# Performance work log

Measured on AMD Instinct MI355X. Metric: run time of the kernel, lower is better.

Reference implementation:

```python
import jax, jax.numpy as jnp
import numpy as np

NUM_CLASSES = 100000   # vocab (input_dim of the layer)
DIM = 256              # embedding dim (output_dim of the layer)
BATCH = 256
NUM_TRUE = 1024        # hardcoded num_true in call()
NUM_SAMPLED = 16384    # hardcoded num_sampled in call()
LOG_RANGE = float(np.log(NUM_CLASSES + 1.0))


def _sample_log_uniform_unique(rng, n, range_max):
    # Mimics tf log_uniform_candidate_sampler with unique=True: rejection-sample
    # from P(c) ~ log((c+2)/(c+1)) until n unique ids are collected.
    seen = {}
    log_range = np.log(range_max + 1.0)
    while len(seen) < n:
        u = rng.uniform(0.0, log_range, size=2 * n)
        ids = np.minimum(np.floor(np.exp(u) - 1.0).astype(np.int64), range_max - 1)
        for v in ids.tolist():
            if len(seen) >= n:
                break
            seen[v] = None
    return np.fromiter(seen.keys(), dtype=np.int64, count=n)


def setup_inputs() -> dict:
    key = jax.random.key(0)
    k1, k2, k3, k4 = jax.random.split(key, 4)
    inputs = jax.random.normal(k1, (BATCH, DIM), jnp.float32)
    # Original inits w/b to zeros; use small random values for a non-degenerate baseline.
    w = jax.random.normal(k2, (NUM_CLASSES, DIM), jnp.float32) * 0.02
    b = jax.random.normal(k3, (NUM_CLASSES,), jnp.float32) * 0.02
    labels = jax.random.randint(k4, (BATCH, NUM_TRUE), 0, NUM_CLASSES, dtype=jnp.int32)
    rng = np.random.default_rng(0)
    sampled = jnp.asarray(_sample_log_uniform_unique(rng, NUM_SAMPLED, NUM_CLASSES), jnp.int32)
    return {"inputs": inputs, "w": w, "b": b, "labels": labels, "sampled": sampled}


def _log_uniform_prob(ids):
    idf = ids.astype(jnp.float32)
    return jnp.log((idf + 2.0) / (idf + 1.0)) / LOG_RANGE


def _expected_count(ids):
    # P(id appears among NUM_SAMPLED unique candidates) = 1 - (1-p)^NUM_SAMPLED
    p = _log_uniform_prob(ids)
    return -jnp.expm1(NUM_SAMPLED * jnp.log1p(-p))


def _sigmoid_xent(logits, target):
    # numerically stable sigmoid cross-entropy, target is a scalar label value
    return jnp.maximum(logits, 0.0) - logits * target + jnp.log1p(jnp.exp(-jnp.abs(logits)))


def reference(inputs, w, b, labels, sampled):
    # true logits: per-example dot with each true class row  [B, T]
    true_w = w[labels]                                    # [B, T, D] gather
    true_logits = jnp.einsum('bd,btd->bt', inputs, true_w) + b[labels]
    true_logits = true_logits - jnp.log(_expected_count(labels))
    # sampled logits: shared candidate set  [B, S]
    sampled_logits = inputs @ w[sampled].T + b[sampled]
    sampled_logits = sampled_logits - jnp.log(_expected_count(sampled))
    # NCE targets: 1/num_true for true classes, 0 for sampled; sum over columns
    true_xent = _sigmoid_xent(true_logits, 1.0 / NUM_TRUE)
    sampled_xent = _sigmoid_xent(sampled_logits, 0.0)
    return true_xent.sum(axis=1) + sampled_xent.sum(axis=1)   # [B]
```

## Files before the change

kernel.cpp:

```cpp
#include <hip/hip_runtime.h>
#include <hip/hip_bf16.h>

#define NUM_CLASSES 100000
#define DIM 256
#define BATCH 256
#define NUM_TRUE 1024
#define NUM_SAMPLED 16384
#define LOG_RANGE 11.51293546492023f
#define INV_LOG_RANGE (1.0f / LOG_RANGE)

#define SBLOCKS 512
#define TBLOCKS 2048

typedef __bf16 bf16x8 __attribute__((ext_vector_type(8)));
typedef float  f32x4  __attribute__((ext_vector_type(4)));

static __device__ __forceinline__ unsigned short f2bf(float f) {
    unsigned int u = __float_as_uint(f);
    unsigned int lsb = (u >> 16) & 1u;
    u += 0x7fffu + lsb;
    return (unsigned short)(u >> 16);
}

static __device__ __forceinline__ float neg_log_ec_fast(int id) {
    float idf = (float)id;
    float e = 1.0f / (idf + 1.0f);
    float p = log1pf(e) * INV_LOG_RANGE;
    float q = p * (1.0f + 0.5f * p + 0.3333333f * p * p);
    float ec = 1.0f - __expf(-(float)NUM_SAMPLED * q);
    return -__logf(ec);
}

static __device__ __forceinline__ float dot4(float4 a, float4 b) {
    return fmaf(a.x, b.x, fmaf(a.y, b.y, fmaf(a.z, b.z, a.w * b.w)));
}

__global__ __launch_bounds__(256) void conv_kernel(const float* __restrict__ in,
                                                   unsigned short* __restrict__ out) {
    int idx = blockIdx.x * 256 + threadIdx.x;
    float4 v = ((const float4*)in)[idx];
    ushort4 p;
    p.x = f2bf(v.x); p.y = f2bf(v.y); p.z = f2bf(v.z); p.w = f2bf(v.w);
    ((ushort4*)out)[idx] = p;
}

__global__ __launch_bounds__(256) void fused_kernel(const float* __restrict__ inputs,
                                                    const float* __restrict__ w,
                                                    const float* __restrict__ bias,
                                                    const int* __restrict__ labels,
                                                    const int* __restrict__ sampled,
                                                    const unsigned short* __restrict__ inbf,
                                                    float* __restrict__ truep,
                                                    float* __restrict__ partial) {
    __shared__ unsigned short lw[32][264];
    __shared__ float cs[32];
    __shared__ float bacc[BATCH];
    __shared__ __align__(16) float ins[DIM];
    __shared__ float wsum[4];

    const int tid = threadIdx.x;

    if (blockIdx.x < SBLOCKS) {
        const int sblk = blockIdx.x;
        const int s0 = sblk * 32;
        bacc[tid] = 0.0f;

        const int inner = tid & 15;
        const int r16   = tid >> 4;
        #pragma unroll
        for (int rb = 0; rb < 2; ++rb) {
            const int r = rb * 16 + r16;
            const int id = sampled[s0 + r];
            const float* src = w + (size_t)id * DIM;
            #pragma unroll
            for (int j = 0; j < 4; ++j) {
                float4 v = *(const float4*)(src + j * 64 + inner * 4);
                ushort4 pk;
                pk.x = f2bf(v.x); pk.y = f2bf(v.y); pk.z = f2bf(v.z); pk.w = f2bf(v.w);
                *(ushort4*)(&lw[r][j * 64 + inner * 4]) = pk;
            }
        }
        if (tid < 32) {
            const int id = sampled[s0 + tid];
            cs[tid] = bias[id] + neg_log_ec_fast(id);
        }
        __syncthreads();

        const int lane = tid & 63;
        const int wv   = tid >> 6;
        const int m    = lane & 15;
        const int quad = lane >> 4;
        const int shalf = (wv >> 1) * 16;
        const int bhalf = (wv & 1) * 128;

        bf16x8 af[8];
        #pragma unroll
        for (int kk = 0; kk < 8; ++kk)
            af[kk] = *(const bf16x8*)(&lw[shalf + m][kk * 32 + quad * 8]);

        #pragma unroll
        for (int t = 0; t < 8; ++t) {
            const int brow = bhalf + t * 16 + m;
            const unsigned short* bp = inbf + brow * DIM;
            bf16x8 bf[8];
            #pragma unroll
            for (int kk = 0; kk < 8; ++kk)
                bf[kk] = *(const bf16x8*)(bp + kk * 32 + quad * 8);
            f32x4 acc = {0, 0, 0, 0};
            #pragma unroll
            for (int kk = 0; kk < 8; ++kk)
                acc = __builtin_amdgcn_mfma_f32_16x16x32_bf16(af[kk], bf[kk], acc, 0, 0, 0);
            float ps = 0.0f;
            #pragma unroll
            for (int r = 0; r < 4; ++r) {
                float c = cs[shalf + quad * 4 + r];
                float l = acc[r] + c;
                ps += fmaxf(l, 0.0f) + __logf(1.0f + __expf(-fabsf(l)));
            }
            ps += __shfl_xor(ps, 16); ps += __shfl_xor(ps, 32);
            if (quad == 0) atomicAdd(&bacc[bhalf + t * 16 + m], ps);
        }
        __syncthreads();
        partial[tid * SBLOCKS + sblk] = bacc[tid];
    } else {
        const int bid  = blockIdx.x - SBLOCKS;
        const int b    = bid >> 3;
        const int chnk = bid & 7;
        ins[tid] = inputs[b * DIM + tid];
        __syncthreads();

        const int lane = tid & 63;
        const int wv   = tid >> 6;
        const int sub  = lane >> 4;
        const int part = lane & 15;
        const float4* ir = (const float4*)ins;
        const float4 in0 = ir[part], in1 = ir[16 + part], in2 = ir[32 + part], in3 = ir[48 + part];

        const int* lab = labels + b * NUM_TRUE + chnk * 128 + wv * 32;

        float4 buf[2][4];
        float  cb[2];
        #pragma unroll
        for (int s = 0; s < 2; ++s) {
            int l = lab[s * 4 + sub];
            const float4* wr = (const float4*)(w + (size_t)l * DIM);
            buf[s][0] = wr[part];      buf[s][1] = wr[16 + part];
            buf[s][2] = wr[32 + part]; buf[s][3] = wr[48 + part];
            cb[s] = bias[l] + neg_log_ec_fast(l);
        }

        float acc = 0.0f;
        #pragma unroll
        for (int i = 0; i < 8; ++i) {
            const int cur = i & 1;
            float4 w0 = buf[cur][0], w1 = buf[cur][1], w2 = buf[cur][2], w3 = buf[cur][3];
            float cl = cb[cur];
            if (i < 6) {
                int l = lab[(i + 2) * 4 + sub];
                const float4* wr = (const float4*)(w + (size_t)l * DIM);
                buf[cur][0] = wr[part];      buf[cur][1] = wr[16 + part];
                buf[cur][2] = wr[32 + part]; buf[cur][3] = wr[48 + part];
                cb[cur] = bias[l] + neg_log_ec_fast(l);
            }
            float d = dot4(w0, in0) + dot4(w1, in1) + dot4(w2, in2) + dot4(w3, in3);
            d += __shfl_xor(d, 1); d += __shfl_xor(d, 2);
            d += __shfl_xor(d, 4); d += __shfl_xor(d, 8);
            float logit = d + cl;
            float v = fmaxf(logit, 0.0f) - logit * (1.0f / (float)NUM_TRUE)
                    + __logf(1.0f + __expf(-fabsf(logit)));
            acc += (part == 0) ? v : 0.0f;
        }
        acc += __shfl_xor(acc, 16); acc += __shfl_xor(acc, 32);
        if (lane == 0) wsum[wv] = acc;
        __syncthreads();
        if (tid == 0) truep[b * 8 + chnk] = wsum[0] + wsum[1] + wsum[2] + wsum[3];
    }
}

__global__ __launch_bounds__(256) void reduce_kernel(const float* __restrict__ partial,
                                                     const float* __restrict__ truep,
                                                     float* __restrict__ out) {
    __shared__ float wsum[4];
    const int b = blockIdx.x;
    const int tid = threadIdx.x;
    float v = partial[b * SBLOCKS + tid] + partial[b * SBLOCKS + 256 + tid];
    if (tid < 8) v += truep[b * 8 + tid];
    v += __shfl_xor(v, 1);  v += __shfl_xor(v, 2);  v += __shfl_xor(v, 4);
    v += __shfl_xor(v, 8);  v += __shfl_xor(v, 16); v += __shfl_xor(v, 32);
    if ((tid & 63) == 0) wsum[tid >> 6] = v;
    __syncthreads();
    if (tid == 0) out[b] = wsum[0] + wsum[1] + wsum[2] + wsum[3];
}

extern "C" void kernel_launch(void* const* d_in, const int* in_sizes, int n_in,
                              void* d_out, int out_size, void* d_ws, size_t ws_size,
                              hipStream_t stream) {
    const float* inputs  = (const float*)d_in[0];
    const float* w       = (const float*)d_in[1];
    const float* bias    = (const float*)d_in[2];
    const int*   labels  = (const int*)d_in[3];
    const int*   sampled = (const int*)d_in[4];
    float* out = (float*)d_out;

    unsigned short* inbf    = (unsigned short*)d_ws;
    float*          truep   = (float*)((char*)d_ws + 131072);
    float*          partial = (float*)((char*)d_ws + 139264);

    conv_kernel<<<64, 256, 0, stream>>>(inputs, inbf);
    fused_kernel<<<SBLOCKS + TBLOCKS, 256, 0, stream>>>(inputs, w, bias, labels,
                                                        sampled, inbf, truep, partial);
    reduce_kernel<<<BATCH, 256, 0, stream>>>(partial, truep, out);
}
```

Measured before the change: 181.4 us.

## Invert true-logit gather into per-class buckets streaming each weight row once

Adds a scatter pass that counts label occurrences per class and records which batch rows use each class, capped at 32 entries per class. The true-logit blocks then stream the weight matrix class by class and dot each row with the input rows that reference it. This replaces the 256K random weight-row gathers with one sequential pass over the table. The cost is atomic contention on the counts, a memset, and serial per-class dot loops. Any class used more than 32 times would be silently truncated, which is safe only for the expected label distribution.

```diff
diff --git a/kernel.cpp b/kernel.cpp
--- a/kernel.cpp
+++ b/kernel.cpp
@@ -10,7 +10,10 @@
 #define INV_LOG_RANGE (1.0f / LOG_RANGE)
 
 #define SBLOCKS 512
-#define TBLOCKS 2048
+#define WBLOCKS 512
+#define CPB 196
+#define CPW 49
+#define CAP 32
 
 typedef __bf16 bf16x8 __attribute__((ext_vector_type(8)));
 typedef float  f32x4  __attribute__((ext_vector_type(4)));
@@ -35,28 +38,36 @@
     return fmaf(a.x, b.x, fmaf(a.y, b.y, fmaf(a.z, b.z, a.w * b.w)));
 }
 
-__global__ __launch_bounds__(256) void conv_kernel(const float* __restrict__ in,
-                                                   unsigned short* __restrict__ out) {
-    int idx = blockIdx.x * 256 + threadIdx.x;
-    float4 v = ((const float4*)in)[idx];
-    ushort4 p;
-    p.x = f2bf(v.x); p.y = f2bf(v.y); p.z = f2bf(v.z); p.w = f2bf(v.w);
-    ((ushort4*)out)[idx] = p;
+__global__ __launch_bounds__(256) void scatter_kernel(const int* __restrict__ labels,
+                                                      const float* __restrict__ inputs,
+                                                      int* __restrict__ counts,
+                                                      unsigned char* __restrict__ bucket,
+                                                      unsigned short* __restrict__ inbf) {
+    const int gid = blockIdx.x * 256 + threadIdx.x;
+    const int c = labels[gid];
+    const int b = gid >> 10;
+    int pos = atomicAdd(&counts[c], 1);
+    if (pos < CAP) bucket[c * CAP + pos] = (unsigned char)b;
+    if (gid < (BATCH * DIM) / 4) {
+        float4 v = ((const float4*)inputs)[gid];
+        ushort4 p;
+        p.x = f2bf(v.x); p.y = f2bf(v.y); p.z = f2bf(v.z); p.w = f2bf(v.w);
+        ((ushort4*)inbf)[gid] = p;
+    }
 }
 
 __global__ __launch_bounds__(256) void fused_kernel(const float* __restrict__ inputs,
                                                     const float* __restrict__ w,
                                                     const float* __restrict__ bias,
-                                                    const int* __restrict__ labels,
                                                     const int* __restrict__ sampled,
+                                                    const int* __restrict__ counts,
+                                                    const unsigned char* __restrict__ bucket,
                                                     const unsigned short* __restrict__ inbf,
-                                                    float* __restrict__ truep,
-                                                    float* __restrict__ partial) {
+                                                    float* __restrict__ partialS,
+                                                    float* __restrict__ partialT) {
     __shared__ unsigned short lw[32][264];
     __shared__ float cs[32];
     __shared__ float bacc[BATCH];
-    __shared__ __align__(16) float ins[DIM];
-    __shared__ float wsum[4];
 
     const int tid = threadIdx.x;
 
@@ -121,70 +132,79 @@
             if (quad == 0) atomicAdd(&bacc[bhalf + t * 16 + m], ps);
         }
         __syncthreads();
-        partial[tid * SBLOCKS + sblk] = bacc[tid];
+        partialS[tid * SBLOCKS + sblk] = bacc[tid];
     } else {
-        const int bid  = blockIdx.x - SBLOCKS;
-        const int b    = bid >> 3;
-        const int chnk = bid & 7;
-        ins[tid] = inputs[b * DIM + tid];
+        const int swblk = blockIdx.x - SBLOCKS;
+        bacc[tid] = 0.0f;
         __syncthreads();
 
         const int lane = tid & 63;
         const int wv   = tid >> 6;
-        const int sub  = lane >> 4;
-        const int part = lane & 15;
-        const float4* ir = (const float4*)ins;
-        const float4 in0 = ir[part], in1 = ir[16 + part], in2 = ir[32 + part], in3 = ir[48 + part];
-
-        const int* lab = labels + b * NUM_TRUE + chnk * 128 + wv * 32;
-
-        float4 buf[2][4];
-        float  cb[2];
+        const int c0   = swblk * CPB + wv * CPW;
+
+        float4 row[2]; int cnt[2]; float bs[2]; int be[2];
         #pragma unroll
         for (int s = 0; s < 2; ++s) {
-            int l = lab[s * 4 + sub];
-            const float4* wr = (const float4*)(w + (size_t)l * DIM);
-            buf[s][0] = wr[part];      buf[s][1] = wr[16 + part];
-            buf[s][2] = wr[32 + part]; buf[s][3] = wr[48 + part];
-            cb[s] = bias[l] + neg_log_ec_fast(l);
-        }
-
-        float acc = 0.0f;
-        #pragma unroll
-        for (int i = 0; i < 8; ++i) {
+            const int c = c0 + s;
+            const int cc = (c < NUM_CLASSES) ? c : (NUM_CLASSES - 1);
+            row[s] = ((const float4*)(w + (size_t)cc * DIM))[lane];
+            cnt[s] = (c < NUM_CLASSES) ? counts[cc] : 0;
+            bs[s]  = bias[cc];
+            be[s]  = bucket[cc * CAP + (lane & 31)];
+        }
+
+        for (int i = 0; i < CPW; ++i) {
             const int cur = i & 1;
-            float4 w0 = buf[cur][0], w1 = buf[cur][1], w2 = buf[cur][2], w3 = buf[cur][3];
-            float cl = cb[cur];
-            if (i < 6) {
-                int l = lab[(i + 2) * 4 + sub];
-                const float4* wr = (const float4*)(w + (size_t)l * DIM);
-                buf[cur][0] = wr[part];      buf[cur][1] = wr[16 + part];
-                buf[cur][2] = wr[32 + part]; buf[cur][3] = wr[48 + part];
-                cb[cur] = bias[l] + neg_log_ec_fast(l);
-            }
-            float d = dot4(w0, in0) + dot4(w1, in1) + dot4(w2, in2) + dot4(w3, in3);
-            d += __shfl_xor(d, 1); d += __shfl_xor(d, 2);
-            d += __shfl_xor(d, 4); d += __shfl_xor(d, 8);
-            float logit = d + cl;
-            float v = fmaxf(logit, 0.0f) - logit * (1.0f / (float)NUM_TRUE)
-                    + __logf(1.0f + __expf(-fabsf(logit)));
-            acc += (part == 0) ? v : 0.0f;
-        }
-        acc += __shfl_xor(acc, 16); acc += __shfl_xor(acc, 32);
-        if (lane == 0) wsum[wv] = acc;
-        __syncthreads();
-        if (tid == 0) truep[b * 8 + chnk] = wsum[0] + wsum[1] + wsum[2] + wsum[3];
+            const float4 wr = row[cur];
+            int n = cnt[cur];
+            const float bv = bs[cur];
+            const int bent = be[cur];
+            const int c = c0 + i;
+            if (i + 2 < CPW) {
+                const int c2 = c0 + i + 2;
+                const int cc = (c2 < NUM_CLASSES) ? c2 : (NUM_CLASSES - 1);
+                row[cur] = ((const float4*)(w + (size_t)cc * DIM))[lane];
+                cnt[cur] = (c2 < NUM_CLASSES) ? counts[cc] : 0;
+                bs[cur]  = bias[cc];
+                be[cur]  = bucket[cc * CAP + (lane & 31)];
+            }
+            if (n > 0) {
+                if (n > CAP) n = CAP;
+                const float cl = bv + neg_log_ec_fast(c);
+                int b0 = __shfl(bent, 0);
+                float4 iv = ((const float4*)(inputs + b0 * DIM))[lane];
+                for (int j = 0; j < n; ++j) {
+                    const int bb = __shfl(bent, j);
+                    float4 ivn = {0, 0, 0, 0};
+                    if (j + 1 < n) {
+                        const int bn = __shfl(bent, j + 1);
+                        ivn = ((const float4*)(inputs + bn * DIM))[lane];
+                    }
+                    float d = dot4(wr, iv);
+                    d += __shfl_xor(d, 1);  d += __shfl_xor(d, 2);
+                    d += __shfl_xor(d, 4);  d += __shfl_xor(d, 8);
+                    d += __shfl_xor(d, 16); d += __shfl_xor(d, 32);
+                    const float logit = d + cl;
+                    const float v = fmaxf(logit, 0.0f) - logit * (1.0f / (float)NUM_TRUE)
+                                  + __logf(1.0f + __expf(-fabsf(logit)));
+                    if (lane == 0) atomicAdd(&bacc[bb], v);
+                    iv = ivn;
+                }
+            }
+        }
+        __syncthreads();
+        partialT[tid * WBLOCKS + swblk] = bacc[tid];
     }
 }
 
-__global__ __launch_bounds__(256) void reduce_kernel(const float* __restrict__ partial,
-                                                     const float* __restrict__ truep,
+__global__ __launch_bounds__(256) void reduce_kernel(const float* __restrict__ partialS,
+                                                     const float* __restrict__ partialT,
                                                      float* __restrict__ out) {
     __shared__ float wsum[4];
     const int b = blockIdx.x;
     const int tid = threadIdx.x;
-    float v = partial[b * SBLOCKS + tid] + partial[b * SBLOCKS + 256 + tid];
-    if (tid < 8) v += truep[b * 8 + tid];
+    float v = partialS[b * SBLOCKS + tid] + partialS[b * SBLOCKS + 256 + tid]
+            + partialT[b * WBLOCKS + tid] + partialT[b * WBLOCKS + 256 + tid];
     v += __shfl_xor(v, 1);  v += __shfl_xor(v, 2);  v += __shfl_xor(v, 4);
     v += __shfl_xor(v, 8);  v += __shfl_xor(v, 16); v += __shfl_xor(v, 32);
     if ((tid & 63) == 0) wsum[tid >> 6] = v;
@@ -202,12 +222,17 @@
     const int*   sampled = (const int*)d_in[4];
     float* out = (float*)d_out;
 
-    unsigned short* inbf    = (unsigned short*)d_ws;
-    float*          truep   = (float*)((char*)d_ws + 131072);
-    float*          partial = (float*)((char*)d_ws + 139264);
-
-    conv_kernel<<<64, 256, 0, stream>>>(inputs, inbf);
-    fused_kernel<<<SBLOCKS + TBLOCKS, 256, 0, stream>>>(inputs, w, bias, labels,
-                                                        sampled, inbf, truep, partial);
-    reduce_kernel<<<BATCH, 256, 0, stream>>>(partial, truep, out);
-}
+    int*            counts   = (int*)d_ws;
+    unsigned char*  bucket   = (unsigned char*)d_ws + 409600;
+    unsigned short* inbf     = (unsigned short*)((char*)d_ws + 3612672);
+    float*          partialS = (float*)((char*)d_ws + 3743744);
+    float*          partialT = (float*)((char*)d_ws + 4268032);
+
+    hipMemsetAsync(counts, 0, NUM_CLASSES * sizeof(int), stream);
+    scatter_kernel<<<(BATCH * NUM_TRUE) / 256, 256, 0, stream>>>(labels, inputs,
+                                                                 counts, bucket, inbf);
+    fused_kernel<<<SBLOCKS + WBLOCKS, 256, 0, stream>>>(inputs, w, bias, sampled,
+                                                        counts, bucket, inbf,
+                                                        partialS, partialT);
+    reduce_kernel<<<BATCH, 256, 0, stream>>>(partialS, partialT, out);
+}
```

After: 299.2 us. 1.65x slower.

## Replace per-label row gathers with a dense class sweep using packed label counts

Applied to the files above, without the earlier changes.

The per-example gather of 1024 true-class weight rows is removed. A scatter kernel builds a per-class table of 4-bit label counts per batch row, plus a sampled-membership flag and a bf16 copy of the inputs. A sweep kernel then reads every weight row once and computes all class-by-batch logits with bf16 MFMA. Each logit is weighted by its label count and sampled flag inside the cross-entropy sum. This trades random 1 KB row gathers for one streaming pass over the weight matrix plus a 13 MB memset and atomics. It also adds two risks: true-class logits now use bf16 instead of fp32, and a class appearing more than 15 times in one batch row would overflow its nibble.

```diff
diff --git a/kernel.cpp b/kernel.cpp
--- a/kernel.cpp
+++ b/kernel.cpp
@@ -2,18 +2,18 @@
 #include <hip/hip_bf16.h>
 
 #define NUM_CLASSES 100000
+#define CLS_PAD 102400
 #define DIM 256
 #define BATCH 256
 #define NUM_TRUE 1024
 #define NUM_SAMPLED 16384
 #define LOG_RANGE 11.51293546492023f
 #define INV_LOG_RANGE (1.0f / LOG_RANGE)
-
-#define SBLOCKS 512
-#define TBLOCKS 2048
+#define SWEEP_BLOCKS 1600
 
 typedef __bf16 bf16x8 __attribute__((ext_vector_type(8)));
 typedef float  f32x4  __attribute__((ext_vector_type(4)));
+typedef unsigned short us8 __attribute__((ext_vector_type(8)));
 
 static __device__ __forceinline__ unsigned short f2bf(float f) {
     unsigned int u = __float_as_uint(f);
@@ -31,160 +31,125 @@
     return -__logf(ec);
 }
 
-static __device__ __forceinline__ float dot4(float4 a, float4 b) {
-    return fmaf(a.x, b.x, fmaf(a.y, b.y, fmaf(a.z, b.z, a.w * b.w)));
-}
-
-__global__ __launch_bounds__(256) void conv_kernel(const float* __restrict__ in,
-                                                   unsigned short* __restrict__ out) {
-    int idx = blockIdx.x * 256 + threadIdx.x;
-    float4 v = ((const float4*)in)[idx];
-    ushort4 p;
-    p.x = f2bf(v.x); p.y = f2bf(v.y); p.z = f2bf(v.z); p.w = f2bf(v.w);
-    ((ushort4*)out)[idx] = p;
-}
-
-__global__ __launch_bounds__(256) void fused_kernel(const float* __restrict__ inputs,
-                                                    const float* __restrict__ w,
-                                                    const float* __restrict__ bias,
-                                                    const int* __restrict__ labels,
-                                                    const int* __restrict__ sampled,
-                                                    const unsigned short* __restrict__ inbf,
-                                                    float* __restrict__ truep,
-                                                    float* __restrict__ partial) {
-    __shared__ unsigned short lw[32][264];
-    __shared__ float cs[32];
-    __shared__ float bacc[BATCH];
-    __shared__ __align__(16) float ins[DIM];
-    __shared__ float wsum[4];
-
-    const int tid = threadIdx.x;
-
-    if (blockIdx.x < SBLOCKS) {
-        const int sblk = blockIdx.x;
-        const int s0 = sblk * 32;
-        bacc[tid] = 0.0f;
-
-        const int inner = tid & 15;
-        const int r16   = tid >> 4;
-        #pragma unroll
-        for (int rb = 0; rb < 2; ++rb) {
-            const int r = rb * 16 + r16;
-            const int id = sampled[s0 + r];
-            const float* src = w + (size_t)id * DIM;
-            #pragma unroll
-            for (int j = 0; j < 4; ++j) {
-                float4 v = *(const float4*)(src + j * 64 + inner * 4);
-                ushort4 pk;
-                pk.x = f2bf(v.x); pk.y = f2bf(v.y); pk.z = f2bf(v.z); pk.w = f2bf(v.w);
-                *(ushort4*)(&lw[r][j * 64 + inner * 4]) = pk;
-            }
-        }
-        if (tid < 32) {
-            const int id = sampled[s0 + tid];
-            cs[tid] = bias[id] + neg_log_ec_fast(id);
-        }
-        __syncthreads();
-
-        const int lane = tid & 63;
-        const int wv   = tid >> 6;
-        const int m    = lane & 15;
-        const int quad = lane >> 4;
-        const int shalf = (wv >> 1) * 16;
-        const int bhalf = (wv & 1) * 128;
-
-        bf16x8 af[8];
-        #pragma unroll
-        for (int kk = 0; kk < 8; ++kk)
-            af[kk] = *(const bf16x8*)(&lw[shalf + m][kk * 32 + quad * 8]);
-
-        #pragma unroll
-        for (int t = 0; t < 8; ++t) {
-            const int brow = bhalf + t * 16 + m;
-            const unsigned short* bp = inbf + brow * DIM;
-            bf16x8 bf[8];
-            #pragma unroll
-            for (int kk = 0; kk < 8; ++kk)
-                bf[kk] = *(const bf16x8*)(bp + kk * 32 + quad * 8);
-            f32x4 acc = {0, 0, 0, 0};
-            #pragma unroll
-            for (int kk = 0; kk < 8; ++kk)
-                acc = __builtin_amdgcn_mfma_f32_16x16x32_bf16(af[kk], bf[kk], acc, 0, 0, 0);
-            float ps = 0.0f;
-            #pragma unroll
-            for (int r = 0; r < 4; ++r) {
-                float c = cs[shalf + quad * 4 + r];
-                float l = acc[r] + c;
-                ps += fmaxf(l, 0.0f) + __logf(1.0f + __expf(-fabsf(l)));
-            }
-            ps += __shfl_xor(ps, 16); ps += __shfl_xor(ps, 32);
-            if (quad == 0) atomicAdd(&bacc[bhalf + t * 16 + m], ps);
-        }
-        __syncthreads();
-        partial[tid * SBLOCKS + sblk] = bacc[tid];
-    } else {
-        const int bid  = blockIdx.x - SBLOCKS;
-        const int b    = bid >> 3;
-        const int chnk = bid & 7;
-        ins[tid] = inputs[b * DIM + tid];
-        __syncthreads();
-
-        const int lane = tid & 63;
-        const int wv   = tid >> 6;
-        const int sub  = lane >> 4;
-        const int part = lane & 15;
-        const float4* ir = (const float4*)ins;
-        const float4 in0 = ir[part], in1 = ir[16 + part], in2 = ir[32 + part], in3 = ir[48 + part];
-
-        const int* lab = labels + b * NUM_TRUE + chnk * 128 + wv * 32;
-
-        float4 buf[2][4];
-        float  cb[2];
-        #pragma unroll
-        for (int s = 0; s < 2; ++s) {
-            int l = lab[s * 4 + sub];
-            const float4* wr = (const float4*)(w + (size_t)l * DIM);
-            buf[s][0] = wr[part];      buf[s][1] = wr[16 + part];
-            buf[s][2] = wr[32 + part]; buf[s][3] = wr[48 + part];
-            cb[s] = bias[l] + neg_log_ec_fast(l);
-        }
-
-        float acc = 0.0f;
-        #pragma unroll
-        for (int i = 0; i < 8; ++i) {
-            const int cur = i & 1;
-            float4 w0 = buf[cur][0], w1 = buf[cur][1], w2 = buf[cur][2], w3 = buf[cur][3];
-            float cl = cb[cur];
-            if (i < 6) {
-                int l = lab[(i + 2) * 4 + sub];
-                const float4* wr = (const float4*)(w + (size_t)l * DIM);
-                buf[cur][0] = wr[part];      buf[cur][1] = wr[16 + part];
-                buf[cur][2] = wr[32 + part]; buf[cur][3] = wr[48 + part];
-                cb[cur] = bias[l] + neg_log_ec_fast(l);
-            }
-            float d = dot4(w0, in0) + dot4(w1, in1) + dot4(w2, in2) + dot4(w3, in3);
-            d += __shfl_xor(d, 1); d += __shfl_xor(d, 2);
-            d += __shfl_xor(d, 4); d += __shfl_xor(d, 8);
-            float logit = d + cl;
-            float v = fmaxf(logit, 0.0f) - logit * (1.0f / (float)NUM_TRUE)
-                    + __logf(1.0f + __expf(-fabsf(logit)));
-            acc += (part == 0) ? v : 0.0f;
-        }
-        acc += __shfl_xor(acc, 16); acc += __shfl_xor(acc, 32);
-        if (lane == 0) wsum[wv] = acc;
-        __syncthreads();
-        if (tid == 0) truep[b * 8 + chnk] = wsum[0] + wsum[1] + wsum[2] + wsum[3];
+__global__ __launch_bounds__(256) void scatter_kernel(const int* __restrict__ labels,
+                                                      const int* __restrict__ sampled,
+                                                      const float* __restrict__ inputs,
+                                                      unsigned int* __restrict__ table,
+                                                      unsigned char* __restrict__ flags,
+                                                      unsigned short* __restrict__ inbf) {
+    const int gid = blockIdx.x * 256 + threadIdx.x;
+    const int c = labels[gid];
+    const int b = gid >> 10;
+    atomicAdd(&table[c * 32 + (b >> 3)], 1u << ((b & 7) * 4));
+    if (gid < NUM_SAMPLED) flags[sampled[gid]] = 1;
+    if (gid < (BATCH * DIM) / 4) {
+        float4 v = ((const float4*)inputs)[gid];
+        ushort4 p;
+        p.x = f2bf(v.x); p.y = f2bf(v.y); p.z = f2bf(v.z); p.w = f2bf(v.w);
+        ((ushort4*)inbf)[gid] = p;
     }
 }
 
+__global__ __launch_bounds__(128) void sweep_kernel(const float* __restrict__ w,
+                                                    const float* __restrict__ bias,
+                                                    const unsigned int* __restrict__ table,
+                                                    const unsigned char* __restrict__ flags,
+                                                    const unsigned short* __restrict__ inbf,
+                                                    float* __restrict__ partial) {
+    __shared__ unsigned int lmask[64][32];
+    __shared__ float cs[64];
+    __shared__ float sf[64];
+    __shared__ float bacc[BATCH];
+
+    const int tid = threadIdx.x;
+    const int c0  = blockIdx.x * 64;
+
+    {
+        const int4* src = (const int4*)(table + (size_t)c0 * 32);
+        int4* dst = (int4*)&lmask[0][0];
+        #pragma unroll
+        for (int j = 0; j < 4; ++j) dst[j * 128 + tid] = src[j * 128 + tid];
+    }
+    if (tid < 64) {
+        const int c = c0 + tid;
+        const int cc = (c < NUM_CLASSES) ? c : (NUM_CLASSES - 1);
+        cs[tid] = bias[cc] + neg_log_ec_fast(c);
+        sf[tid] = flags[c] ? 1.0f : 0.0f;
+    }
+    bacc[tid] = 0.0f; bacc[tid + 128] = 0.0f;
+
+    const int lane = tid & 63;
+    const int wv   = tid >> 6;
+    const int m    = lane & 15;
+    const int quad = lane >> 4;
+
+    bf16x8 af[2][8];
+    #pragma unroll
+    for (int s = 0; s < 2; ++s) {
+        int c = c0 + wv * 32 + s * 16 + m;
+        if (c >= NUM_CLASSES) c = NUM_CLASSES - 1;
+        const float* wr = w + (size_t)c * DIM + quad * 8;
+        #pragma unroll
+        for (int kk = 0; kk < 8; ++kk) {
+            float4 v0 = *(const float4*)(wr + kk * 32);
+            float4 v1 = *(const float4*)(wr + kk * 32 + 4);
+            union { us8 u; bf16x8 b; } t;
+            t.u[0] = f2bf(v0.x); t.u[1] = f2bf(v0.y); t.u[2] = f2bf(v0.z); t.u[3] = f2bf(v0.w);
+            t.u[4] = f2bf(v1.x); t.u[5] = f2bf(v1.y); t.u[6] = f2bf(v1.z); t.u[7] = f2bf(v1.w);
+            af[s][kk] = t.b;
+        }
+    }
+    __syncthreads();
+
+    const int cbase = wv * 32;
+    for (int t = 0; t < 16; ++t) {
+        const unsigned short* bp = inbf + (t * 16 + m) * DIM + quad * 8;
+        bf16x8 bf[8];
+        #pragma unroll
+        for (int kk = 0; kk < 8; ++kk) bf[kk] = *(const bf16x8*)(bp + kk * 32);
+        f32x4 a0 = {0, 0, 0, 0}, a1 = {0, 0, 0, 0};
+        #pragma unroll
+        for (int kk = 0; kk < 8; ++kk) {
+            a0 = __builtin_amdgcn_mfma_f32_16x16x32_bf16(af[0][kk], bf[kk], a0, 0, 0, 0);
+            a1 = __builtin_amdgcn_mfma_f32_16x16x32_bf16(af[1][kk], bf[kk], a1, 0, 0, 0);
+        }
+        const int wofs = t * 2 + (m >> 3);
+        const int nsh  = (m & 7) * 4;
+        float ps = 0.0f;
+        #pragma unroll
+        for (int r = 0; r < 4; ++r) {
+            {
+                const int cl = cbase + quad * 4 + r;
+                float l = a0[r] + cs[cl];
+                float kf = (float)((lmask[cl][wofs] >> nsh) & 15u);
+                float base = fmaxf(l, 0.0f) + __logf(1.0f + __expf(-fabsf(l)));
+                ps += (kf + sf[cl]) * base - kf * l * (1.0f / (float)NUM_TRUE);
+            }
+            {
+                const int cl = cbase + 16 + quad * 4 + r;
+                float l = a1[r] + cs[cl];
+                float kf = (float)((lmask[cl][wofs] >> nsh) & 15u);
+                float base = fmaxf(l, 0.0f) + __logf(1.0f + __expf(-fabsf(l)));
+                ps += (kf + sf[cl]) * base - kf * l * (1.0f / (float)NUM_TRUE);
+            }
+        }
+        ps += __shfl_xor(ps, 16); ps += __shfl_xor(ps, 32);
+        if (quad == 0) atomicAdd(&bacc[t * 16 + m], ps);
+    }
+    __syncthreads();
+    partial[blockIdx.x * BATCH + tid]       = bacc[tid];
+    partial[blockIdx.x * BATCH + 128 + tid] = bacc[128 + tid];
+}
+
 __global__ __launch_bounds__(256) void reduce_kernel(const float* __restrict__ partial,
-                                                     const float* __restrict__ truep,
                                                      float* __restrict__ out) {
     __shared__ float wsum[4];
     const int b = blockIdx.x;
     const int tid = threadIdx.x;
-    float v = partial[b * SBLOCKS + tid] + partial[b * SBLOCKS + 256 + tid];
-    if (tid < 8) v += truep[b * 8 + tid];
+    float v = 0.0f;
+    #pragma unroll
+    for (int j = 0; j < 6; ++j) v += partial[(j * 256 + tid) * BATCH + b];
+    if (tid < SWEEP_BLOCKS - 1536) v += partial[(1536 + tid) * BATCH + b];
     v += __shfl_xor(v, 1);  v += __shfl_xor(v, 2);  v += __shfl_xor(v, 4);
     v += __shfl_xor(v, 8);  v += __shfl_xor(v, 16); v += __shfl_xor(v, 32);
     if ((tid & 63) == 0) wsum[tid >> 6] = v;
@@ -202,12 +167,14 @@
     const int*   sampled = (const int*)d_in[4];
     float* out = (float*)d_out;
 
-    unsigned short* inbf    = (unsigned short*)d_ws;
-    float*          truep   = (float*)((char*)d_ws + 131072);
-    float*          partial = (float*)((char*)d_ws + 139264);
+    unsigned int*   table   = (unsigned int*)d_ws;
+    unsigned char*  flags   = (unsigned char*)d_ws + 13107200;
+    unsigned short* inbf    = (unsigned short*)((char*)d_ws + 13209600);
+    float*          partial = (float*)((char*)d_ws + 13340672);
 
-    conv_kernel<<<64, 256, 0, stream>>>(inputs, inbf);
-    fused_kernel<<<SBLOCKS + TBLOCKS, 256, 0, stream>>>(inputs, w, bias, labels,
-                                                        sampled, inbf, truep, partial);
-    reduce_kernel<<<BATCH, 256, 0, stream>>>(partial, truep, out);
+    hipMemsetAsync(table, 0, 13209600, stream);
+    scatter_kernel<<<(BATCH * NUM_TRUE) / 256, 256, 0, stream>>>(labels, sampled, inputs,
+                                                                 table, flags, inbf);
+    sweep_kernel<<<SWEEP_BLOCKS, 128, 0, stream>>>(w, bias, table, flags, inbf, partial);
+    reduce_kernel<<<BATCH, 256, 0, stream>>>(partial, out);
 }
```

Result: slower. 236.8 us (+30.5%).
